# Kernel optimization log

Hardware: AMD Instinct MI355X
Metric: run time of the kernel (lower is better)

Reference implementation:

```python
import jax, jax.numpy as jnp
import numpy as np

NUM_CLASS = 15
STRIDES = (8, 16, 32)
SCALE_FACTOR = 2.0
DELTA = 0.01
DELTA_CONF = 0.01
EPS = 1e-6


def bce_logits(x, t):
    # numerically stable BCEWithLogits, reduction='none'
    return jnp.maximum(x, 0.0) - x * t + jnp.log1p(jnp.exp(-jnp.abs(x)))


def focal(x, t, gamma=2.0, alpha=1.0):
    return alpha * bce_logits(x, t) * jnp.abs(t - jax.nn.sigmoid(x)) ** gamma


def smooth_l1(x, t):
    # torch SmoothL1Loss default beta=1.0, reduction='none'
    n = jnp.abs(x - t)
    return jnp.where(n < 1.0, 0.5 * n * n, n - 0.5)


def giou_xywh(b1, b2):
    # xywh (center) -> xyxy, order-fixed, standard GIOU (utils_basic.GIOU_xywh_torch)
    b1 = jnp.concatenate([b1[..., :2] - b1[..., 2:4] * 0.5, b1[..., :2] + b1[..., 2:4] * 0.5], -1)
    b2 = jnp.concatenate([b2[..., :2] - b2[..., 2:4] * 0.5, b2[..., :2] + b2[..., 2:4] * 0.5], -1)
    b1 = jnp.concatenate([jnp.minimum(b1[..., :2], b1[..., 2:]), jnp.maximum(b1[..., :2], b1[..., 2:])], -1)
    b2 = jnp.concatenate([jnp.minimum(b2[..., :2], b2[..., 2:]), jnp.maximum(b2[..., :2], b2[..., 2:])], -1)
    a1 = (b1[..., 2] - b1[..., 0]) * (b1[..., 3] - b1[..., 1])
    a2 = (b2[..., 2] - b2[..., 0]) * (b2[..., 3] - b2[..., 1])
    lt = jnp.maximum(b1[..., :2], b2[..., :2])
    rb = jnp.minimum(b1[..., 2:], b2[..., 2:])
    wh = jnp.clip(rb - lt, 0.0)
    inter = wh[..., 0] * wh[..., 1]
    union = a1 + a2 - inter
    iou = inter / (union + EPS)
    elt = jnp.minimum(b1[..., :2], b2[..., :2])
    erb = jnp.maximum(b1[..., 2:], b2[..., 2:])
    ewh = jnp.clip(erb - elt, 0.0)
    enclose = ewh[..., 0] * ewh[..., 1]
    return iou - (enclose - union) / (enclose + EPS)


def cal_loss(p1, p1_d, p2, p2_d, label, stride):
    sg = jax.lax.stop_gradient
    batch_size, grid = p1.shape[0], p1.shape[1]
    img_size = float(stride * grid)
    label_xywh = label[..., :4]
    label_l1234 = label[..., 4:8]
    label_a = label[..., 8:12]
    label_r = label[..., 12:13]
    label_mix = label[..., 14:15]
    label_cls = label[..., 16:]

    obj_mask = (label[..., 13:14] == 1).astype(jnp.float32)
    noobj_mask = 1.0 - (label[..., 13:14] != 0).astype(jnp.float32)
    fuzzy_mask = 1.0 - obj_mask - noobj_mask
    gh = jnp.max(label_cls, axis=-1, keepdims=True)

    label_conf_smooth = obj_mask * (1.0 - DELTA_CONF) + DELTA_CONF / 2.0
    cls_nz = (label_cls != 0).astype(jnp.float32)
    label_cls_smooth = cls_nz * (1.0 - DELTA) + DELTA / NUM_CLASS
    area_weight = label[..., 15:16] + (label[..., 15:16] == 0).astype(jnp.float32)
    bbox_loss_scale = SCALE_FACTOR - (SCALE_FACTOR - 1.0) * label_xywh[..., 2:3] * label_xywh[..., 3:4] / (img_size * img_size)

    N = jnp.sum(obj_mask.reshape(batch_size, -1), axis=-1) + 1e-16
    N = jnp.maximum(N, 1.0).reshape(batch_size, 1, 1, 1)

    # ---------------- head 1 ----------------
    p1_d_xywh, p1_d_s, p1_d_r, p1_d_l = p1_d[..., :4], p1_d[..., 4:8], p1_d[..., 8:9], p1_d[..., 9:13]
    p1_conf = p1[..., 9:10]
    xiou1 = giou_xywh(p1_d_xywh, label_xywh)[..., None]
    scores_iou1 = bbox_loss_scale * (1.0 - jnp.clip(xiou1, 0.0, 1.0))
    scores_obb1 = jnp.sum((p1_d_s - label_a) ** 2, axis=-1, keepdims=True)
    scores_area1 = (p1_d_r - label_r) ** 2
    scores_loc1 = jnp.exp(-(scores_iou1 + scores_obb1 + scores_area1))
    offset01 = jnp.max(sg(scores_loc1), axis=-1, keepdims=True)
    g1 = (gh + offset01) / 2.0
    bg_mask1 = noobj_mask + fuzzy_mask * (g1 < 0.3).astype(jnp.float32) * (1.0 - fuzzy_mask * g1)
    fg_mask1 = obj_mask * (g1 >= 0.3).astype(jnp.float32)

    loss_fg1 = fg_mask1 * focal(p1_conf, label_conf_smooth) * label_mix * g1
    loss_bg1 = bg_mask1 * focal(p1_conf, label_conf_smooth) * label_mix
    loss_iou1 = fg_mask1 * scores_iou1 * label_mix * area_weight
    loss_s1 = fg_mask1 * scores_obb1 * label_mix * area_weight
    loss_r1 = fg_mask1 * scores_area1 * label_mix * area_weight
    loss_l1 = fg_mask1 * bbox_loss_scale * smooth_l1(p1_d_l / stride, label_l1234 / stride) * label_mix * area_weight

    loss_fg1 = jnp.sum(loss_fg1 / N) / batch_size * 2
    loss_bg1 = jnp.sum(loss_bg1 / N) / batch_size * 2
    loss_iou1 = jnp.sum(loss_iou1 / N) / batch_size
    loss_s1 = jnp.sum(loss_s1 / N) / batch_size
    loss_r1 = 16 * jnp.sum(loss_r1 / N) / batch_size
    loss_l1 = 0.2 * jnp.sum(loss_l1 / N) / batch_size

    # ---------------- head 2 ----------------
    p2_d_xywh, p2_d_s, p2_d_r, p2_d_l = p2_d[..., :4], p2_d[..., 4:8], p2_d[..., 8:9], p2_d[..., 9:13]
    p2_conf = p2[..., 9:10]
    p2_cls = p2[..., 10:]
    xiou2 = giou_xywh(p2_d_xywh, label_xywh)[..., None]
    scores_iou2 = bbox_loss_scale * (1.0 - jnp.clip(xiou2, 0.0, 1.0))
    scores_obb2 = jnp.sum((p2_d_s - label_a) ** 2, axis=-1, keepdims=True)
    scores_area2 = (p2_d_r - label_r) ** 2
    offset02 = sg(jnp.exp(-(scores_iou2 + scores_obb2 + scores_area2)))
    g2 = (gh + offset02) / 2.0
    bg_mask2 = noobj_mask + fuzzy_mask * (g2 < 0.3).astype(jnp.float32) * (1.0 - fuzzy_mask * g2)
    fg_mask2 = obj_mask * (g2 >= 0.3).astype(jnp.float32)

    loss_fg2 = fg_mask2 * focal(p2_conf, label_conf_smooth) * label_mix * g2
    loss_bg2 = bg_mask2 * focal(p2_conf, label_conf_smooth) * label_mix
    loss_pos2 = cls_nz * obj_mask * bce_logits(p2_cls, label_cls_smooth * offset02) * label_mix * area_weight
    loss_neg2 = (1.0 - cls_nz) * obj_mask * bce_logits(p2_cls, label_cls_smooth) * label_mix * area_weight
    weight_cls2 = jnp.sum(cls_nz * jax.nn.sigmoid(sg(p2_cls)), axis=-1, keepdims=True)
    wg = (weight_cls2 + gh) / 2.0
    loss_iou2 = fg_mask2 * scores_iou2 * label_mix * area_weight * wg
    loss_s2 = fg_mask2 * scores_obb2 * label_mix * area_weight * wg
    loss_r2 = fg_mask2 * scores_area2 * label_mix * area_weight * wg
    loss_l2 = fg_mask2 * bbox_loss_scale * smooth_l1(p2_d_l / stride, label_l1234 / stride) * label_mix * area_weight * wg
    loss_cls2 = fg_mask2 * bce_logits(p2_cls, label_cls_smooth) * label_mix * area_weight

    loss_fg2 = jnp.sum(loss_fg2 / N) / batch_size * 2
    loss_bg2 = jnp.sum(loss_bg2 / N) / batch_size * 2
    loss_pos2 = jnp.sum(loss_pos2 / N) / batch_size * (NUM_CLASS - 1)
    loss_neg2 = jnp.sum(loss_neg2 / N) / batch_size
    loss_iou2 = jnp.sum(loss_iou2 / N) / batch_size
    loss_cls2 = jnp.sum(loss_cls2 / N) / batch_size
    loss_s2 = jnp.sum(loss_s2 / N) / batch_size
    loss_r2 = 16 * jnp.sum(loss_r2 / N) / batch_size
    loss_l2 = 0.2 * jnp.sum(loss_l2 / N) / batch_size

    loss_fg = (loss_fg1 + loss_fg2) / 2
    loss_bg = (loss_bg1 + loss_bg2) / 2
    loss_pos = loss_pos2 * 2
    loss_neg = loss_neg2 * 2
    loss_cls = loss_cls2
    loss_iou = (loss_iou1 + loss_iou2) / 2
    loss_s = (loss_s1 + loss_s2) / 2
    loss_r = (loss_r1 + loss_r2) / 2
    loss_l = (loss_l1 + loss_l2) / 2
    loss = loss_fg + loss_bg + loss_iou + (loss_s + loss_r) + loss_pos + loss_neg + loss_l
    return (loss, loss_fg, loss_bg, loss_pos, loss_neg, loss_iou, loss_cls, loss_s, loss_r, loss_l)


def _make_label(key, B, G, stride):
    ks = jax.random.split(key, 7)
    img = float(G * stride)
    xywh = jax.random.uniform(ks[0], (B, G, G, 4), minval=1.0, maxval=img)
    l1234 = jax.random.uniform(ks[1], (B, G, G, 4), minval=0.0, maxval=img)
    a = jax.random.uniform(ks[2], (B, G, G, 4))
    r = jax.random.uniform(ks[3], (B, G, G, 1))
    flag = jax.random.randint(ks[4], (B, G, G, 1), 0, 3).astype(jnp.float32) / 2.0  # {0,0.5,1}
    mix_area = jax.random.uniform(ks[5], (B, G, G, 2))
    cls_k1, cls_k2 = jax.random.split(ks[6])
    cls = jax.random.uniform(cls_k1, (B, G, G, NUM_CLASS)) * (jax.random.uniform(cls_k2, (B, G, G, NUM_CLASS)) < 0.1)
    return jnp.concatenate([xywh, l1234, a, r, flag, mix_area, cls], -1)


def setup_inputs() -> dict:
    key = jax.random.key(0)
    B = 16
    grids = (128, 64, 32)
    inp = {}
    names = ('s', 'm', 'l')
    for idx, (G, stride, nm) in enumerate(zip(grids, STRIDES, names)):
        ks = jax.random.split(jax.random.fold_in(key, idx), 5)
        inp['p1_' + nm] = jax.random.normal(ks[0], (B, G, G, 10), jnp.float32)
        inp['p1d_' + nm] = jax.random.uniform(ks[1], (B, G, G, 13), minval=0.0, maxval=float(G * stride))
        inp['p2_' + nm] = jax.random.normal(ks[2], (B, G, G, 25), jnp.float32)
        inp['p2d_' + nm] = jax.random.uniform(ks[3], (B, G, G, 13), minval=0.0, maxval=float(G * stride))
        inp['label_' + nm] = _make_label(ks[4], B, G, stride)
    inp['epoch'] = 10
    inp['i'] = 100
    return inp


def reference(p1_s, p1_m, p1_l, p1d_s, p1d_m, p1d_l, p2_s, p2_m, p2_l, p2d_s, p2d_m, p2d_l, label_s, label_m, label_l, epoch, i):
    outs = [
        cal_loss(p1_s, p1d_s, p2_s, p2d_s, label_s, STRIDES[0]),
        cal_loss(p1_m, p1d_m, p2_m, p2d_m, label_m, STRIDES[1]),
        cal_loss(p1_l, p1d_l, p2_l, p2d_l, label_l, STRIDES[2]),
    ]
    totals = [outs[0][k] + outs[1][k] + outs[2][k] for k in range(10)]
    return jnp.stack(totals)  # [loss, fg, bg, pos, neg, iou, cls, s, r, l]
```

## Files before the change

### kernel.cpp

```cpp
#include <hip/hip_runtime.h>
#include <math.h>

#define NC 15

typedef float f4_t __attribute__((ext_vector_type(4)));
typedef f4_t __attribute__((aligned(4))) u4_t;
typedef float f2_t __attribute__((ext_vector_type(2)));
typedef f2_t __attribute__((aligned(4))) u2_t;

struct Params {
    const float* p1[3];
    const float* p1d[3];
    const float* p2[3];
    const float* p2d[3];
    const float* lb[3];
    double* sums;
};

__device__ __forceinline__ float rcp_f(float x) { return __builtin_amdgcn_rcpf(x); }

__device__ __forceinline__ float focal_f(float x, float t) {
    float e = __expf(-fabsf(x));
    float rc = rcp_f(1.0f + e);
    float sp = __logf(1.0f + e);
    float bce = fmaxf(x, 0.0f) - x * t + sp;
    float sig = (x >= 0.0f ? 1.0f : e) * rc;
    float d = t - sig;
    return bce * d * d;
}
__device__ __forceinline__ float sl1_f(float x, float t) {
    float n = fabsf(x - t);
    return n < 1.0f ? 0.5f * n * n : n - 0.5f;
}

__device__ __forceinline__ float giou_f(f4_t b, float lx, float ly, float lw, float lh) {
    float b1x0 = b.x - b.z * 0.5f, b1y0 = b.y - b.w * 0.5f;
    float b1x1 = b.x + b.z * 0.5f, b1y1 = b.y + b.w * 0.5f;
    float b2x0 = lx - lw * 0.5f, b2y0 = ly - lh * 0.5f;
    float b2x1 = lx + lw * 0.5f, b2y1 = ly + lh * 0.5f;
    float ax0 = fminf(b1x0, b1x1), ay0 = fminf(b1y0, b1y1);
    float ax1 = fmaxf(b1x0, b1x1), ay1 = fmaxf(b1y0, b1y1);
    float cx0 = fminf(b2x0, b2x1), cy0 = fminf(b2y0, b2y1);
    float cx1 = fmaxf(b2x0, b2x1), cy1 = fmaxf(b2y0, b2y1);
    float a1 = (ax1 - ax0) * (ay1 - ay0);
    float a2 = (cx1 - cx0) * (cy1 - cy0);
    float ltx = fmaxf(ax0, cx0), lty = fmaxf(ay0, cy0);
    float rbx = fminf(ax1, cx1), rby = fminf(ay1, cy1);
    float iw = fmaxf(rbx - ltx, 0.0f), ih = fmaxf(rby - lty, 0.0f);
    float inter = iw * ih;
    float uni = a1 + a2 - inter;
    float iou = inter * rcp_f(uni + 1e-6f);
    float ex0 = fminf(ax0, cx0), ey0 = fminf(ay0, cy0);
    float ex1 = fmaxf(ax1, cx1), ey1 = fmaxf(ay1, cy1);
    float ew = fmaxf(ex1 - ex0, 0.0f), eh = fmaxf(ey1 - ey0, 0.0f);
    float enc = ew * eh;
    return iou - (enc - uni) * rcp_f(enc + 1e-6f);
}

__global__ __launch_bounds__(256, 5) void loss_all(Params P) {
    __shared__ float red[4][10];

    int tid = threadIdx.x;
    int bid = blockIdx.x;
    int lvl, lblk, shift;
    float invStride;
    if (bid >= 1280)      { lvl = 2; lblk = bid - 1280; shift = 10; invStride = 1.0f / 32.0f; }
    else if (bid >= 1024) { lvl = 1; lblk = bid - 1024; shift = 12; invStride = 1.0f / 16.0f; }
    else                  { lvl = 0; lblk = bid;        shift = 14; invStride = 1.0f / 8.0f;  }
    int c = (lblk << 8) + tid;
    int batch = c >> shift;

    const float* lb = P.lb[lvl] + (size_t)c * 31;
    u4_t L0 = *(const u4_t*)(lb + 0);
    u4_t L1 = *(const u4_t*)(lb + 4);
    u4_t L2 = *(const u4_t*)(lb + 8);
    u4_t L3 = *(const u4_t*)(lb + 12);
    u4_t L4 = *(const u4_t*)(lb + 16);
    u4_t L5 = *(const u4_t*)(lb + 20);
    u4_t L6 = *(const u4_t*)(lb + 24);
    u2_t L7 = *(const u2_t*)(lb + 28);
    float c14 = lb[30];

    const float* pa = P.p1d[lvl] + (size_t)c * 13;
    u4_t A0 = *(const u4_t*)(pa + 0);
    u4_t A1 = *(const u4_t*)(pa + 4);
    u4_t A2 = *(const u4_t*)(pa + 8);
    float A3 = pa[12];

    const float* pb = P.p2d[lvl] + (size_t)c * 13;
    u4_t B0 = *(const u4_t*)(pb + 0);
    u4_t B1 = *(const u4_t*)(pb + 4);
    u4_t B2 = *(const u4_t*)(pb + 8);
    float B3 = pb[12];

    const float* pq = P.p2[lvl] + (size_t)c * 25 + 9;
    u4_t Q0 = *(const u4_t*)(pq + 0);
    u4_t Q1 = *(const u4_t*)(pq + 4);
    u4_t Q2 = *(const u4_t*)(pq + 8);
    u4_t Q3 = *(const u4_t*)(pq + 12);

    float conf1 = P.p1[lvl][(size_t)c * 10 + 9];

    float lx = L0.x, ly = L0.y, lw = L0.z, lh = L0.w;
    float lr = L3.x, flag = L3.y, mix = L3.z, area = L3.w;
    float cl[NC] = {L4.x, L4.y, L4.z, L4.w, L5.x, L5.y, L5.z, L5.w,
                    L6.x, L6.y, L6.z, L6.w, L7.x, L7.y, c14};
    float gh = 0.0f;
    unsigned nzm = 0u;
#pragma unroll
    for (int k = 0; k < NC; ++k) {
        gh = fmaxf(gh, cl[k]);
        if (cl[k] != 0.0f) nzm |= (1u << k);
    }
    float obj   = (flag == 1.0f) ? 1.0f : 0.0f;
    float noobj = (flag == 0.0f) ? 1.0f : 0.0f;
    float fuzzy = 1.0f - obj - noobj;
    float conf_t = obj * 0.99f + 0.005f;
    float aw = area + ((area == 0.0f) ? 1.0f : 0.0f);
    float bls = 2.0f - lw * lh * (1.0f / (1024.0f * 1024.0f));

    float v0, v1, v2, v3, v4, v5, v6, v7, v8, v9;

    {
        float xiou = giou_f(A0, lx, ly, lw, lh);
        float siou = bls * (1.0f - fminf(fmaxf(xiou, 0.0f), 1.0f));
        float d0 = A1.x - L2.x, d1 = A1.y - L2.y, d2 = A1.z - L2.z, d3 = A1.w - L2.w;
        float sobb = d0 * d0 + d1 * d1 + d2 * d2 + d3 * d3;
        float dr = A2.x - lr;
        float sarea = dr * dr;
        float off = __expf(-(siou + sobb + sarea));
        float g = (gh + off) * 0.5f;
        float bg = noobj + fuzzy * ((g < 0.3f) ? 1.0f : 0.0f) * (1.0f - fuzzy * g);
        float fg = obj * ((g >= 0.3f) ? 1.0f : 0.0f);
        float foc = focal_f(conf1, conf_t);
        float fma_ = fg * mix * aw;
        v0 = fg * foc * mix * g;
        v1 = bg * foc * mix;
        v2 = fma_ * siou;
        v3 = fma_ * sobb;
        v4 = fma_ * sarea;
        float sl = sl1_f(A2.y * invStride, L1.x * invStride)
                 + sl1_f(A2.z * invStride, L1.y * invStride)
                 + sl1_f(A2.w * invStride, L1.z * invStride)
                 + sl1_f(A3 * invStride,   L1.w * invStride);
        v5 = fg * bls * sl * mix * aw;
    }

    {
        float xiou = giou_f(B0, lx, ly, lw, lh);
        float siou2 = bls * (1.0f - fminf(fmaxf(xiou, 0.0f), 1.0f));
        float d0 = B1.x - L2.x, d1 = B1.y - L2.y, d2 = B1.z - L2.z, d3 = B1.w - L2.w;
        float sobb2 = d0 * d0 + d1 * d1 + d2 * d2 + d3 * d3;
        float dr = B2.x - lr;
        float sarea2 = dr * dr;
        float off2 = __expf(-(siou2 + sobb2 + sarea2));
        float sl2 = sl1_f(B2.y * invStride, L1.x * invStride)
                  + sl1_f(B2.z * invStride, L1.y * invStride)
                  + sl1_f(B2.w * invStride, L1.z * invStride)
                  + sl1_f(B3 * invStride,   L1.w * invStride);

        float conf2 = Q0.x;
        float g = (gh + off2) * 0.5f;
        float bg = noobj + fuzzy * ((g < 0.3f) ? 1.0f : 0.0f) * (1.0f - fuzzy * g);
        float fg = obj * ((g >= 0.3f) ? 1.0f : 0.0f);
        float foc = focal_f(conf2, conf_t);
        v0 += fg * foc * mix * g;
        v1 += bg * foc * mix;

        float cx[NC] = {Q0.y, Q0.z, Q0.w, Q1.x, Q1.y, Q1.z, Q1.w,
                        Q2.x, Q2.y, Q2.z, Q2.w, Q3.x, Q3.y, Q3.z, Q3.w};
        float pos = 0.0f, neg = 0.0f, wsum = 0.0f, clsb = 0.0f;
#pragma unroll
        for (int k = 0; k < NC; ++k) {
            float x = cx[k];
            bool nz = (nzm >> k) & 1u;
            float smn = (nz ? 0.99f : 0.0f) + (0.01f / 15.0f);
            float e = __expf(-fabsf(x));
            float sp = __logf(1.0f + e);
            float mx = fmaxf(x, 0.0f);
            float b0 = mx - x * smn + sp;
            clsb += b0;
            if (nz) {
                pos += mx - x * (smn * off2) + sp;
                wsum += (x >= 0.0f ? 1.0f : e) * rcp_f(1.0f + e);
            } else {
                neg += b0;
            }
        }
        float wgq = (wsum + gh) * 0.5f;
        float oma = obj * mix * aw;
        v6 = oma * pos;
        v7 = oma * neg;
        float fmaw = fg * mix * aw * wgq;
        v2 += fmaw * siou2;
        v3 += fmaw * sobb2;
        v4 += fmaw * sarea2;
        v5 += fg * bls * sl2 * mix * aw * wgq;
        v8 = fg * clsb * mix * aw;
    }
    v9 = obj;

#pragma unroll
    for (int o = 32; o > 0; o >>= 1) {
        v0 += __shfl_down(v0, o);
        v1 += __shfl_down(v1, o);
        v2 += __shfl_down(v2, o);
        v3 += __shfl_down(v3, o);
        v4 += __shfl_down(v4, o);
        v5 += __shfl_down(v5, o);
        v6 += __shfl_down(v6, o);
        v7 += __shfl_down(v7, o);
        v8 += __shfl_down(v8, o);
        v9 += __shfl_down(v9, o);
    }
    int lane = tid & 63, wid = tid >> 6;
    if (lane == 0) {
        red[wid][0] = v0; red[wid][1] = v1; red[wid][2] = v2; red[wid][3] = v3;
        red[wid][4] = v4; red[wid][5] = v5; red[wid][6] = v6; red[wid][7] = v7;
        red[wid][8] = v8; red[wid][9] = v9;
    }
    __syncthreads();
    if (tid < 10) {
        float total = red[0][tid] + red[1][tid] + red[2][tid] + red[3][tid];
        atomicAdd(&P.sums[((size_t)((lvl << 4) + batch)) * 10 + tid], (double)total);
    }
}

__global__ __launch_bounds__(64) void finalize_kernel(const double* __restrict__ S,
                                                      float* __restrict__ out) {
    int lane = threadIdx.x;
    double loc[10];
#pragma unroll
    for (int t = 0; t < 10; ++t) loc[t] = 0.0;
    if (lane < 48) {
        const double* s = S + (size_t)lane * 10;
        double invN = 1.0 / fmax(s[9], 1.0);
#pragma unroll
        for (int t = 0; t < 9; ++t) loc[t] = s[t] * invN;
    }
#pragma unroll
    for (int t = 0; t < 9; ++t) {
#pragma unroll
        for (int o = 32; o > 0; o >>= 1) loc[t] += __shfl_down(loc[t], o);
    }
    if (lane == 0) {
        const double invB = 1.0 / 16.0;
        double fg  = loc[0] * invB;
        double bg  = loc[1] * invB;
        double iou = loc[2] * invB * 0.5;
        double s_  = loc[3] * invB * 0.5;
        double r   = loc[4] * invB * 8.0;
        double l   = loc[5] * invB * 0.1;
        double pos = loc[6] * invB * 28.0;
        double neg = loc[7] * invB * 2.0;
        double cls = loc[8] * invB;
        double loss = fg + bg + iou + s_ + r + pos + neg + l;
        out[0] = (float)loss; out[1] = (float)fg; out[2] = (float)bg;
        out[3] = (float)pos;  out[4] = (float)neg; out[5] = (float)iou;
        out[6] = (float)cls;  out[7] = (float)s_;  out[8] = (float)r;
        out[9] = (float)l;
    }
}

extern "C" void kernel_launch(void* const* d_in, const int* in_sizes, int n_in,
                              void* d_out, int out_size, void* d_ws, size_t ws_size,
                              hipStream_t stream) {
    (void)in_sizes; (void)n_in; (void)out_size; (void)ws_size;
    double* sums = (double*)d_ws;
    hipMemsetAsync(d_ws, 0, 48 * 10 * sizeof(double), stream);

    Params P;
    for (int lvl = 0; lvl < 3; ++lvl) {
        P.p1[lvl]  = (const float*)d_in[lvl * 5 + 0];
        P.p1d[lvl] = (const float*)d_in[lvl * 5 + 1];
        P.p2[lvl]  = (const float*)d_in[lvl * 5 + 2];
        P.p2d[lvl] = (const float*)d_in[lvl * 5 + 3];
        P.lb[lvl]  = (const float*)d_in[lvl * 5 + 4];
    }
    P.sums = sums;

    loss_all<<<dim3(1344), dim3(256), 0, stream>>>(P);
    finalize_kernel<<<dim3(1), dim3(64), 0, stream>>>(sums, (float*)d_out);
}
```

Measured before the change: 39.18 us.

## Split loss kernel into per-head blocks to double parallelism and cut registers

```diff
diff --git a/kernel.cpp b/kernel.cpp
--- a/kernel.cpp
+++ b/kernel.cpp
@@ -57,71 +57,57 @@
     return iou - (enc - uni) * rcp_f(enc + 1e-6f);
 }
 
-__global__ __launch_bounds__(256, 5) void loss_all(Params P) {
+__global__ __launch_bounds__(256) void loss_head(Params P) {
     __shared__ float red[4][10];
 
     int tid = threadIdx.x;
     int bid = blockIdx.x;
+    int head = bid & 1;
+    int sub = bid >> 1;
     int lvl, lblk, shift;
     float invStride;
-    if (bid >= 1280)      { lvl = 2; lblk = bid - 1280; shift = 10; invStride = 1.0f / 32.0f; }
-    else if (bid >= 1024) { lvl = 1; lblk = bid - 1024; shift = 12; invStride = 1.0f / 16.0f; }
-    else                  { lvl = 0; lblk = bid;        shift = 14; invStride = 1.0f / 8.0f;  }
+    if (sub >= 1280)      { lvl = 2; lblk = sub - 1280; shift = 10; invStride = 1.0f / 32.0f; }
+    else if (sub >= 1024) { lvl = 1; lblk = sub - 1024; shift = 12; invStride = 1.0f / 16.0f; }
+    else                  { lvl = 0; lblk = sub;        shift = 14; invStride = 1.0f / 8.0f;  }
     int c = (lblk << 8) + tid;
     int batch = c >> shift;
 
+    float v0 = 0.0f, v1 = 0.0f, v2 = 0.0f, v3 = 0.0f, v4 = 0.0f,
+          v5 = 0.0f, v6 = 0.0f, v7 = 0.0f, v8 = 0.0f, v9 = 0.0f;
+
     const float* lb = P.lb[lvl] + (size_t)c * 31;
-    u4_t L0 = *(const u4_t*)(lb + 0);
-    u4_t L1 = *(const u4_t*)(lb + 4);
-    u4_t L2 = *(const u4_t*)(lb + 8);
-    u4_t L3 = *(const u4_t*)(lb + 12);
-    u4_t L4 = *(const u4_t*)(lb + 16);
-    u4_t L5 = *(const u4_t*)(lb + 20);
-    u4_t L6 = *(const u4_t*)(lb + 24);
-    u2_t L7 = *(const u2_t*)(lb + 28);
-    float c14 = lb[30];
-
-    const float* pa = P.p1d[lvl] + (size_t)c * 13;
-    u4_t A0 = *(const u4_t*)(pa + 0);
-    u4_t A1 = *(const u4_t*)(pa + 4);
-    u4_t A2 = *(const u4_t*)(pa + 8);
-    float A3 = pa[12];
-
-    const float* pb = P.p2d[lvl] + (size_t)c * 13;
-    u4_t B0 = *(const u4_t*)(pb + 0);
-    u4_t B1 = *(const u4_t*)(pb + 4);
-    u4_t B2 = *(const u4_t*)(pb + 8);
-    float B3 = pb[12];
-
-    const float* pq = P.p2[lvl] + (size_t)c * 25 + 9;
-    u4_t Q0 = *(const u4_t*)(pq + 0);
-    u4_t Q1 = *(const u4_t*)(pq + 4);
-    u4_t Q2 = *(const u4_t*)(pq + 8);
-    u4_t Q3 = *(const u4_t*)(pq + 12);
-
-    float conf1 = P.p1[lvl][(size_t)c * 10 + 9];
-
-    float lx = L0.x, ly = L0.y, lw = L0.z, lh = L0.w;
-    float lr = L3.x, flag = L3.y, mix = L3.z, area = L3.w;
-    float cl[NC] = {L4.x, L4.y, L4.z, L4.w, L5.x, L5.y, L5.z, L5.w,
-                    L6.x, L6.y, L6.z, L6.w, L7.x, L7.y, c14};
-    float gh = 0.0f;
-    unsigned nzm = 0u;
-#pragma unroll
-    for (int k = 0; k < NC; ++k) {
-        gh = fmaxf(gh, cl[k]);
-        if (cl[k] != 0.0f) nzm |= (1u << k);
-    }
-    float obj   = (flag == 1.0f) ? 1.0f : 0.0f;
-    float noobj = (flag == 0.0f) ? 1.0f : 0.0f;
-    float fuzzy = 1.0f - obj - noobj;
-    float conf_t = obj * 0.99f + 0.005f;
-    float aw = area + ((area == 0.0f) ? 1.0f : 0.0f);
-    float bls = 2.0f - lw * lh * (1.0f / (1024.0f * 1024.0f));
-
-    float v0, v1, v2, v3, v4, v5, v6, v7, v8, v9;
-
-    {
+
+    if (head == 0) {
+        u4_t L0 = *(const u4_t*)(lb + 0);
+        u4_t L1 = *(const u4_t*)(lb + 4);
+        u4_t L2 = *(const u4_t*)(lb + 8);
+        u4_t L3 = *(const u4_t*)(lb + 12);
+        u4_t L4 = *(const u4_t*)(lb + 16);
+        u4_t L5 = *(const u4_t*)(lb + 20);
+        u4_t L6 = *(const u4_t*)(lb + 24);
+        u2_t L7 = *(const u2_t*)(lb + 28);
+        float c14 = lb[30];
+        const float* pa = P.p1d[lvl] + (size_t)c * 13;
+        u4_t A0 = *(const u4_t*)(pa + 0);
+        u4_t A1 = *(const u4_t*)(pa + 4);
+        u4_t A2 = *(const u4_t*)(pa + 8);
+        float A3 = pa[12];
+        float conf1 = P.p1[lvl][(size_t)c * 10 + 9];
+        __builtin_amdgcn_sched_barrier(0);
+
+        float lx = L0.x, ly = L0.y, lw = L0.z, lh = L0.w;
+        float lr = L3.x, flag = L3.y, mix = L3.z, area = L3.w;
+        float gh = fmaxf(fmaxf(fmaxf(L4.x, L4.y), fmaxf(L4.z, L4.w)),
+                   fmaxf(fmaxf(fmaxf(L5.x, L5.y), fmaxf(L5.z, L5.w)),
+                   fmaxf(fmaxf(fmaxf(L6.x, L6.y), fmaxf(L6.z, L6.w)),
+                         fmaxf(fmaxf(L7.x, L7.y), c14))));
+        float obj   = (flag == 1.0f) ? 1.0f : 0.0f;
+        float noobj = (flag == 0.0f) ? 1.0f : 0.0f;
+        float fuzzy = 1.0f - obj - noobj;
+        float conf_t = obj * 0.99f + 0.005f;
+        float aw = area + ((area == 0.0f) ? 1.0f : 0.0f);
+        float bls = 2.0f - lw * lh * (1.0f / (1024.0f * 1024.0f));
+
         float xiou = giou_f(A0, lx, ly, lw, lh);
         float siou = bls * (1.0f - fminf(fmaxf(xiou, 0.0f), 1.0f));
         float d0 = A1.x - L2.x, d1 = A1.y - L2.y, d2 = A1.z - L2.z, d3 = A1.w - L2.w;
@@ -144,9 +130,47 @@
                  + sl1_f(A2.w * invStride, L1.z * invStride)
                  + sl1_f(A3 * invStride,   L1.w * invStride);
         v5 = fg * bls * sl * mix * aw;
-    }
-
-    {
+        v9 = obj;
+    } else {
+        u4_t L0 = *(const u4_t*)(lb + 0);
+        u4_t L1 = *(const u4_t*)(lb + 4);
+        u4_t L2 = *(const u4_t*)(lb + 8);
+        u4_t L3 = *(const u4_t*)(lb + 12);
+        u4_t L4 = *(const u4_t*)(lb + 16);
+        u4_t L5 = *(const u4_t*)(lb + 20);
+        u4_t L6 = *(const u4_t*)(lb + 24);
+        u2_t L7 = *(const u2_t*)(lb + 28);
+        float c14 = lb[30];
+        const float* pb = P.p2d[lvl] + (size_t)c * 13;
+        u4_t B0 = *(const u4_t*)(pb + 0);
+        u4_t B1 = *(const u4_t*)(pb + 4);
+        u4_t B2 = *(const u4_t*)(pb + 8);
+        float B3 = pb[12];
+        const float* pq = P.p2[lvl] + (size_t)c * 25 + 9;
+        u4_t Q0 = *(const u4_t*)(pq + 0);
+        u4_t Q1 = *(const u4_t*)(pq + 4);
+        u4_t Q2 = *(const u4_t*)(pq + 8);
+        u4_t Q3 = *(const u4_t*)(pq + 12);
+        __builtin_amdgcn_sched_barrier(0);
+
+        float lx = L0.x, ly = L0.y, lw = L0.z, lh = L0.w;
+        float lr = L3.x, flag = L3.y, mix = L3.z, area = L3.w;
+        float cl[NC] = {L4.x, L4.y, L4.z, L4.w, L5.x, L5.y, L5.z, L5.w,
+                        L6.x, L6.y, L6.z, L6.w, L7.x, L7.y, c14};
+        float gh = 0.0f;
+        unsigned nzm = 0u;
+#pragma unroll
+        for (int k = 0; k < NC; ++k) {
+            gh = fmaxf(gh, cl[k]);
+            if (cl[k] != 0.0f) nzm |= (1u << k);
+        }
+        float obj   = (flag == 1.0f) ? 1.0f : 0.0f;
+        float noobj = (flag == 0.0f) ? 1.0f : 0.0f;
+        float fuzzy = 1.0f - obj - noobj;
+        float conf_t = obj * 0.99f + 0.005f;
+        float aw = area + ((area == 0.0f) ? 1.0f : 0.0f);
+        float bls = 2.0f - lw * lh * (1.0f / (1024.0f * 1024.0f));
+
         float xiou = giou_f(B0, lx, ly, lw, lh);
         float siou2 = bls * (1.0f - fminf(fmaxf(xiou, 0.0f), 1.0f));
         float d0 = B1.x - L2.x, d1 = B1.y - L2.y, d2 = B1.z - L2.z, d3 = B1.w - L2.w;
@@ -164,8 +188,8 @@
         float bg = noobj + fuzzy * ((g < 0.3f) ? 1.0f : 0.0f) * (1.0f - fuzzy * g);
         float fg = obj * ((g >= 0.3f) ? 1.0f : 0.0f);
         float foc = focal_f(conf2, conf_t);
-        v0 += fg * foc * mix * g;
-        v1 += bg * foc * mix;
+        v0 = fg * foc * mix * g;
+        v1 = bg * foc * mix;
 
         float cx[NC] = {Q0.y, Q0.z, Q0.w, Q1.x, Q1.y, Q1.z, Q1.w,
                         Q2.x, Q2.y, Q2.z, Q2.w, Q3.x, Q3.y, Q3.z, Q3.w};
@@ -192,13 +216,12 @@
         v6 = oma * pos;
         v7 = oma * neg;
         float fmaw = fg * mix * aw * wgq;
-        v2 += fmaw * siou2;
-        v3 += fmaw * sobb2;
-        v4 += fmaw * sarea2;
-        v5 += fg * bls * sl2 * mix * aw * wgq;
+        v2 = fmaw * siou2;
+        v3 = fmaw * sobb2;
+        v4 = fmaw * sarea2;
+        v5 = fg * bls * sl2 * mix * aw * wgq;
         v8 = fg * clsb * mix * aw;
     }
-    v9 = obj;
 
 #pragma unroll
     for (int o = 32; o > 0; o >>= 1) {
@@ -222,7 +245,8 @@
     __syncthreads();
     if (tid < 10) {
         float total = red[0][tid] + red[1][tid] + red[2][tid] + red[3][tid];
-        atomicAdd(&P.sums[((size_t)((lvl << 4) + batch)) * 10 + tid], (double)total);
+        if (total != 0.0f)
+            atomicAdd(&P.sums[((size_t)((lvl << 4) + batch)) * 10 + tid], (double)total);
     }
 }
 
@@ -279,6 +303,6 @@
     }
     P.sums = sums;
 
-    loss_all<<<dim3(1344), dim3(256), 0, stream>>>(P);
+    loss_head<<<dim3(2688), dim3(256), 0, stream>>>(P);
     finalize_kernel<<<dim3(1), dim3(64), 0, stream>>>(sums, (float*)d_out);
 }
```

Result: slower. 40.76 us (+4.0%).
